# Performance work log

Hardware: AMD Instinct MI355X
Metric: run time of the kernel (lower is better)

## Reference

```python
import jax, jax.numpy as jnp
import numpy as np

S = 4096      # total packed sequence length (8 images x 512 patches)
D = 1152      # hidden_dim
H = 16        # num_heads
HD = D // H   # head_dim = 72
MLPD = 4304   # mlp_dim
EPS = 1e-5


def setup_inputs() -> dict:
    key = jax.random.key(0)
    ks = jax.random.split(key, 16)
    f32 = jnp.float32
    w = lambda k, shp: (jax.random.normal(k, shp, f32) * 0.02)
    hidden_states = jax.random.normal(ks[0], (S, D), f32)
    cu_seqlens = (jnp.arange(9, dtype=jnp.int32) * (S // 8))  # [0,512,...,4096]
    angles = jax.random.uniform(ks[1], (S, HD // 2), f32, 0.0, 2.0 * np.pi)
    rope_cos = jnp.cos(angles)
    rope_sin = jnp.sin(angles)
    return {
        "hidden_states": hidden_states,
        "cu_seqlens": cu_seqlens,
        "rope_cos": rope_cos,
        "rope_sin": rope_sin,
        "norm0_scale": jnp.ones((D,), f32),
        "norm0_bias": jnp.zeros((D,), f32),
        "wqkv_w": w(ks[2], (D, 3 * D)),
        "wqkv_b": jnp.zeros((3 * D,), f32),
        "wo_w": w(ks[3], (D, D)),
        "wo_b": jnp.zeros((D,), f32),
        "norm1_scale": jnp.ones((D,), f32),
        "norm1_bias": jnp.zeros((D,), f32),
        "fc0_w": w(ks[4], (D, MLPD)),
        "fc0_b": jnp.zeros((MLPD,), f32),
        "fc1_w": w(ks[5], (MLPD, D)),
        "fc1_b": jnp.zeros((D,), f32),
    }


def _layernorm(x, scale, bias):
    m = jnp.mean(x, axis=-1, keepdims=True)
    v = jnp.mean(jnp.square(x - m), axis=-1, keepdims=True)
    return (x - m) * jax.lax.rsqrt(v + EPS) * scale + bias


def _rope(x, cos, sin):
    # x: (S, H, HD). Complex multiply (x0 + i x1) * (cos + i sin) in real form.
    xr = x.reshape(S, H, HD // 2, 2)
    x0, x1 = xr[..., 0], xr[..., 1]
    c = cos[:, None, :]  # (S, 1, HD/2) broadcast over heads
    s = sin[:, None, :]
    o0 = x0 * c - x1 * s
    o1 = x0 * s + x1 * c
    return jnp.stack([o0, o1], axis=-1).reshape(S, H, HD)


def _block_diag_bias(cu_seqlens):
    positions = jnp.arange(S)
    starts, ends = cu_seqlens[:-1], cu_seqlens[1:]
    in_seg = (positions[:, None] >= starts[None, :]) & (positions[:, None] < ends[None, :])
    seg = jnp.argmax(in_seg.astype(jnp.int32), axis=-1)  # (S,)
    same = seg[:, None] == seg[None, :]
    return jnp.where(same, 0.0, jnp.finfo(jnp.float32).min)  # (S, S)


def reference(hidden_states, cu_seqlens, rope_cos, rope_sin,
              norm0_scale, norm0_bias, wqkv_w, wqkv_b, wo_w, wo_b,
              norm1_scale, norm1_bias, fc0_w, fc0_b, fc1_w, fc1_b):
    # pre-norm attention block
    x = _layernorm(hidden_states, norm0_scale, norm0_bias)
    qkv = (x @ wqkv_w + wqkv_b).reshape(S, 3, H, HD)
    q, k, v = qkv[:, 0], qkv[:, 1], qkv[:, 2]
    q = _rope(q, rope_cos, rope_sin)
    k = _rope(k, rope_cos, rope_sin)
    bias = _block_diag_bias(cu_seqlens)  # (S, S)
    scale = HD ** -0.5
    scores = jnp.einsum('shd,thd->hst', q, k) * scale + bias[None, :, :]
    probs = jax.nn.softmax(scores, axis=-1)
    attn = jnp.einsum('hst,thd->shd', probs, v).reshape(S, D)
    attn = attn @ wo_w + wo_b
    h = hidden_states + attn
    # pre-norm MLP block
    y = _layernorm(h, norm1_scale, norm1_bias)
    y = jax.nn.gelu(y @ fc0_w + fc0_b) @ fc1_w + fc1_b
    return h + y
```

## Files before the change

### kernel.cpp

```cpp
#include <hip/hip_runtime.h>


#define DEV __device__ __forceinline__

typedef __attribute__((ext_vector_type(8))) short short8;
typedef __attribute__((ext_vector_type(4))) float f32x4;

typedef const void __attribute__((address_space(1))) gvoid;
typedef void __attribute__((address_space(3))) lvoid;

DEV ushort f2bf(float f) {
  union { float f; unsigned u; } x; x.f = f;
  unsigned r = (x.u + 0x7FFFu + ((x.u >> 16) & 1u)) >> 16;
  return (ushort)r;
}

DEV float bf2f(ushort u) {
  union { unsigned u; float f; } x; x.u = (unsigned)u << 16;
  return x.f;
}

DEV void gload_lds16(const void* g, void* l) {
  __builtin_amdgcn_global_load_lds((gvoid*)g, (lvoid*)l, 16, 0, 0);
}

DEV f32x4 mfma16(short8 a, short8 b, f32x4 c) {
  return __builtin_amdgcn_mfma_f32_16x16x32_bf16(a, b, c, 0, 0, 0);
}

DEV float gelu_tanh(float x) {
  float x3 = x * x * x;
  return 0.5f * x * (1.f + tanhf(0.7978845608f * (x + 0.044715f * x3)));
}

__global__ void wconv_t(const float* __restrict__ src, ushort* __restrict__ dst,
                        int K, int N, int NP, int KP) {
  __shared__ float tile[32][33];
  const int k0 = blockIdx.x * 32, n0 = blockIdx.y * 32;
  const int tx = threadIdx.x & 31, ty = threadIdx.x >> 5;
#pragma unroll
  for (int i = 0; i < 4; ++i) {
    int r = ty + i * 8;
    float v = 0.f;
    if (k0 + r < K && n0 + tx < N) v = src[(size_t)(k0 + r) * N + n0 + tx];
    tile[tx][r] = v;
  }
  __syncthreads();
#pragma unroll
  for (int i = 0; i < 4; ++i) {
    int r = ty + i * 8;
    dst[(size_t)(n0 + r) * KP + k0 + tx] = f2bf(tile[r][tx]);
  }
}

__global__ __launch_bounds__(256) void ln_bf16(const float* __restrict__ x,
                                               const float* __restrict__ sc,
                                               const float* __restrict__ bi,
                                               ushort* __restrict__ out) {
  const int row = blockIdx.x, tid = threadIdx.x;
  const float* xr = x + (size_t)row * 1152;
  const int n = (tid < 128) ? 5 : 4;
  float vals[5];
  float s = 0.f, s2 = 0.f;
#pragma unroll
  for (int i = 0; i < 5; ++i) {
    if (i < n) { float v = xr[tid + i * 256]; vals[i] = v; s += v; s2 += v * v; }
  }
#pragma unroll
  for (int off = 32; off; off >>= 1) { s += __shfl_xor(s, off); s2 += __shfl_xor(s2, off); }
  __shared__ float rs[4], rs2[4];
  if ((tid & 63) == 0) { rs[tid >> 6] = s; rs2[tid >> 6] = s2; }
  __syncthreads();
  s = rs[0] + rs[1] + rs[2] + rs[3];
  s2 = rs2[0] + rs2[1] + rs2[2] + rs2[3];
  const float mean = s * (1.f / 1152.f);
  const float var = s2 * (1.f / 1152.f) - mean * mean;
  const float rstd = rsqrtf(var + 1e-5f);
  ushort* orow = out + (size_t)row * 1152;
  for (int i = 0; i < n; ++i) {
    int c = tid + i * 256;
    orow[c] = f2bf((vals[i] - mean) * rstd * sc[c] + bi[c]);
  }
}

template <int EPI, int BM>
__global__ __launch_bounds__(BM == 256 ? 512 : 256, 2) void gemm2(
    const ushort* __restrict__ A, const ushort* __restrict__ Bt,
    const float* __restrict__ bias, const float* __restrict__ resid,
    float* __restrict__ outf, ushort* __restrict__ outh,
    int N, int Kstride, int NT, int n_valid) {
  constexpr int T = BM * 2;
  constexpr int NLA = 2;
  constexpr int NLB = 512 / T;
  __shared__ ushort lA[2][BM * 32];
  __shared__ ushort lB[2][128 * 32];
  const int tid = threadIdx.x;
  const int lane = tid & 63, wave = tid >> 6;
  const int l15 = lane & 15, lg = lane >> 4;

  const int nx = gridDim.x, ny = gridDim.y;
  const int nwg = nx * ny * gridDim.z;
  const int hw = (blockIdx.z * ny + blockIdx.y) * nx + blockIdx.x;
  const int F = (hw & 7) * (nwg >> 3) + (hw >> 3);
  const int by = F % ny;
  const int C = F / ny;
  const int bx = C % nx;
  const int bz = C / nx;
  const int m0 = by * BM, n0 = bx * 128;
  const int k0 = bz * NT * 32;

  const int wm = (wave >> 1) * 64;
  const int wn = (wave & 1) * 64;

  const ushort* Asrc[NLA];
  const ushort* Bsrc[NLB];
#pragma unroll
  for (int i = 0; i < NLA; ++i) {
    const int c = i * T + tid;
    const int r = c >> 2, kc = (c & 3) ^ (r & 3);
    Asrc[i] = A + (size_t)(m0 + r) * Kstride + k0 + kc * 8;
  }
#pragma unroll
  for (int j = 0; j < NLB; ++j) {
    const int c = j * T + tid;
    const int r = c >> 2, kc = (c & 3) ^ (r & 3);
    Bsrc[j] = Bt + (size_t)(n0 + r) * Kstride + k0 + kc * 8;
  }

  auto stage = [&](int b, int t) {
#pragma unroll
    for (int i = 0; i < NLA; ++i)
      gload_lds16(Asrc[i] + t * 32, &lA[b][(i * T + wave * 64) * 8]);
#pragma unroll
    for (int j = 0; j < NLB; ++j)
      gload_lds16(Bsrc[j] + t * 32, &lB[b][(j * T + wave * 64) * 8]);
  };

  f32x4 acc[4][4] = {};
  const int cph = (lg ^ (l15 & 3)) * 8;

  stage(0, 0);
  __syncthreads();
  int cur = 0;
  for (int t = 0; t < NT; ++t) {
    if (t + 1 < NT) stage(cur ^ 1, t + 1);
    short8 af[4], bfr[4];
#pragma unroll
    for (int i = 0; i < 4; ++i)
      af[i] = *(const short8*)&lA[cur][(wm + i * 16 + l15) * 32 + cph];
#pragma unroll
    for (int j = 0; j < 4; ++j)
      bfr[j] = *(const short8*)&lB[cur][(wn + j * 16 + l15) * 32 + cph];
#pragma unroll
    for (int i = 0; i < 4; ++i)
#pragma unroll
      for (int j = 0; j < 4; ++j)
        acc[i][j] = mfma16(af[i], bfr[j], acc[i][j]);
    __syncthreads();
    cur ^= 1;
  }

  float* outp = outf;
  if constexpr (EPI == 0) outp = outf + (size_t)bz * 4096 * 1152;
  const int cb = n0 + wn + l15;
  const int rb = m0 + wm + lg * 4;
#pragma unroll
  for (int j = 0; j < 4; ++j) {
    const int col = cb + j * 16;
    const float bv = (EPI != 0 && col < n_valid) ? bias[col] : 0.f;
    const bool ok = (col < n_valid);
#pragma unroll
    for (int i = 0; i < 4; ++i) {
#pragma unroll
      for (int r = 0; r < 4; ++r) {
        const int row = rb + i * 16 + r;
        const size_t idx = (size_t)row * N + col;
        const float v = acc[i][j][r] + bv;
        if constexpr (EPI == 0) outp[idx] = v;
        else if constexpr (EPI == 1) { if (ok) outf[idx] = resid[idx] + v; }
        else if constexpr (EPI == 2) outh[idx] = f2bf(gelu_tanh(v));
        else outh[idx] = f2bf(v);
      }
    }
  }
}

__global__ __launch_bounds__(256) void ksum_reduce(
    const float* __restrict__ hb, const float* __restrict__ bias,
    const float* __restrict__ p0, const float* __restrict__ p1,
    float* __restrict__ out) {
  const f32x4* hb4 = (const f32x4*)hb;
  const f32x4* b4 = (const f32x4*)bias;
  const f32x4* p04 = (const f32x4*)p0;
  const f32x4* p14 = (const f32x4*)p1;
  f32x4* o4 = (f32x4*)out;
  const int total = 4096 * 288;
  for (int i = blockIdx.x * 256 + threadIdx.x; i < total; i += gridDim.x * 256)
    o4[i] = hb4[i] + b4[i % 288] + p04[i] + p14[i];
}

__global__ __launch_bounds__(256) void rope_pack(
    const ushort* __restrict__ qkv,
    const float* __restrict__ cosp, const float* __restrict__ sinp,
    ushort* __restrict__ qp, ushort* __restrict__ kp) {
  const int t = blockIdx.x * 256 + threadIdx.x;
  const int c = t % 12;
  const int hs = t / 12;
  const int h = hs & 15;
  const int s = hs >> 4;
  const size_t dst = ((size_t)h * 4096 + s) * 96 + c * 8;
  if (c >= 9) {
    short8 z = {};
    *(short8*)(qp + dst) = z;
    *(short8*)(kp + dst) = z;
    return;
  }
  const size_t base = (size_t)s * 3456 + h * 72 + c * 8;
  const short8 qv = *(const short8*)(qkv + base);
  const short8 kv = *(const short8*)(qkv + base + 1152);
  const f32x4 cs = *(const f32x4*)(cosp + s * 36 + c * 4);
  const f32x4 sn = *(const f32x4*)(sinp + s * 36 + c * 4);
  short8 qo, ko;
#pragma unroll
  for (int j = 0; j < 4; ++j) {
    const float q0 = bf2f((ushort)qv[2 * j]), q1 = bf2f((ushort)qv[2 * j + 1]);
    const float k0 = bf2f((ushort)kv[2 * j]), k1 = bf2f((ushort)kv[2 * j + 1]);
    qo[2 * j] = (short)f2bf((q0 * cs[j] - q1 * sn[j]) * 0.1178511302f);
    qo[2 * j + 1] = (short)f2bf((q0 * sn[j] + q1 * cs[j]) * 0.1178511302f);
    ko[2 * j] = (short)f2bf(k0 * cs[j] - k1 * sn[j]);
    ko[2 * j + 1] = (short)f2bf(k0 * sn[j] + k1 * cs[j]);
  }
  *(short8*)(qp + dst) = qo;
  *(short8*)(kp + dst) = ko;
}

__global__ void v_pack(const ushort* __restrict__ qkv, ushort* __restrict__ vt) {
  __shared__ ushort lv[96][64];
  const int b = blockIdx.x;
  const int h = b >> 6;
  const int s0 = (b & 63) << 6;
  const int tid = threadIdx.x;
#pragma unroll
  for (int it = 0; it < 24; ++it) {
    int idx = tid + it * 256;
    int d = idx % 96, sl = idx / 96;
    lv[d][sl] = (d < 72) ? qkv[(size_t)(s0 + sl) * 3456 + 2304 + h * 72 + d] : (ushort)0;
  }
  __syncthreads();
#pragma unroll
  for (int it = 0; it < 24; ++it) {
    int idx = tid + it * 256;
    int d = idx >> 6, sl = idx & 63;
    vt[((size_t)h * 96 + d) * 4096 + s0 + sl] = lv[d][sl];
  }
}

__global__ __launch_bounds__(256) void attn_kernel(
    const ushort* __restrict__ qp, const ushort* __restrict__ kp,
    const ushort* __restrict__ vt, ushort* __restrict__ attn_out) {
  __shared__ ushort lp[4][16 * 32];
  const int tid = threadIdx.x, lane = tid & 63, wave = tid >> 6;
  const int l15 = lane & 15, lg = lane >> 4;
  const int b = blockIdx.x;
  const int h = b >> 6;
  const int rem = b & 63;
  const int seg = rem >> 3, qt = rem & 7;
  const int q0 = seg * 512 + qt * 64 + wave * 16;

  short8 aq[3];
  const ushort* qrow = qp + ((size_t)h * 4096 + q0 + l15) * 96 + lg * 8;
  aq[0] = *(const short8*)(qrow);
  aq[1] = *(const short8*)(qrow + 32);
  aq[2] = *(const short8*)(qrow + 64);

  f32x4 oacc[5] = {};
  float mrow[4] = {-1e30f, -1e30f, -1e30f, -1e30f};
  float srow[4] = {0.f, 0.f, 0.f, 0.f};

  const ushort* kbase = kp + ((size_t)h * 4096 + seg * 512) * 96;
  const ushort* vbase = vt + (size_t)h * 96 * 4096 + seg * 512;
  ushort* lpw = lp[wave];

  for (int kc = 0; kc < 16; ++kc) {
    f32x4 sc[2] = {};
#pragma unroll
    for (int n = 0; n < 2; ++n) {
      const ushort* krow = kbase + (size_t)(kc * 32 + n * 16 + l15) * 96 + lg * 8;
#pragma unroll
      for (int c = 0; c < 3; ++c) {
        short8 kb = *(const short8*)(krow + c * 32);
        sc[n] = mfma16(aq[c], kb, sc[n]);
      }
    }
    float corr[4];
#pragma unroll
    for (int j = 0; j < 4; ++j) {
      float v = fmaxf(sc[0][j], sc[1][j]);
      v = fmaxf(v, __shfl_xor(v, 1));
      v = fmaxf(v, __shfl_xor(v, 2));
      v = fmaxf(v, __shfl_xor(v, 4));
      v = fmaxf(v, __shfl_xor(v, 8));
      float mn = fmaxf(mrow[j], v);
      corr[j] = __expf(mrow[j] - mn);
      mrow[j] = mn;
    }
    float p0[4], p1[4];
#pragma unroll
    for (int j = 0; j < 4; ++j) {
      p0[j] = __expf(sc[0][j] - mrow[j]);
      p1[j] = __expf(sc[1][j] - mrow[j]);
      float ps = p0[j] + p1[j];
      ps += __shfl_xor(ps, 1);
      ps += __shfl_xor(ps, 2);
      ps += __shfl_xor(ps, 4);
      ps += __shfl_xor(ps, 8);
      srow[j] = srow[j] * corr[j] + ps;
    }
#pragma unroll
    for (int n = 0; n < 5; ++n)
#pragma unroll
      for (int j = 0; j < 4; ++j)
        oacc[n][j] *= corr[j];
#pragma unroll
    for (int j = 0; j < 4; ++j) {
      int row = lg * 4 + j;
      lpw[row * 32 + l15] = f2bf(p0[j]);
      lpw[row * 32 + 16 + l15] = f2bf(p1[j]);
    }
    __syncthreads();
    short8 pa = *(const short8*)&lpw[l15 * 32 + lg * 8];
    const ushort* vrow = vbase + kc * 32 + lg * 8;
#pragma unroll
    for (int n = 0; n < 5; ++n) {
      short8 vb = *(const short8*)(vrow + (size_t)(n * 16 + l15) * 4096);
      oacc[n] = mfma16(pa, vb, oacc[n]);
    }
    __syncthreads();
  }
#pragma unroll
  for (int j = 0; j < 4; ++j) {
    float inv = 1.f / srow[j];
    int row = q0 + lg * 4 + j;
#pragma unroll
    for (int n = 0; n < 5; ++n) {
      int col = n * 16 + l15;
      if (col < 72)
        attn_out[(size_t)row * 1152 + h * 72 + col] = f2bf(oacc[n][j] * inv);
    }
  }
}

extern "C" void kernel_launch(void* const* d_in, const int* in_sizes, int n_in,
                              void* d_out, int out_size, void* d_ws, size_t ws_size,
                              hipStream_t stream) {
  (void)in_sizes; (void)n_in; (void)out_size;
  const float* hidden = (const float*)d_in[0];
  const float* ropec = (const float*)d_in[2];
  const float* ropes = (const float*)d_in[3];
  const float* n0s = (const float*)d_in[4];
  const float* n0b = (const float*)d_in[5];
  const float* wqkv = (const float*)d_in[6];
  const float* bqkv = (const float*)d_in[7];
  const float* wo = (const float*)d_in[8];
  const float* bo = (const float*)d_in[9];
  const float* n1s = (const float*)d_in[10];
  const float* n1b = (const float*)d_in[11];
  const float* wfc0 = (const float*)d_in[12];
  const float* bfc0 = (const float*)d_in[13];
  const float* wfc1 = (const float*)d_in[14];
  const float* bfc1 = (const float*)d_in[15];
  float* out = (float*)d_out;

  char* ws = (char*)d_ws;
  ushort* x_bf   = (ushort*)(ws + 0);
  ushort* wqkv_t = (ushort*)(ws + 9437184);
  ushort* wo_t   = (ushort*)(ws + 17399808);
  ushort* fc0_t  = (ushort*)(ws + 20054016);
  ushort* fc1_t  = (ushort*)(ws + 30081024);
  ushort* qkv_bf = (ushort*)(ws + 40108032);
  ushort* mid    = (ushort*)(ws + 40108032);
  ushort* q_pad  = (ushort*)(ws + 75759616);
  ushort* k_pad  = (ushort*)(ws + 88342528);
  ushort* vt     = (ushort*)(ws + 100925440);
  float*  pbuf   = (float*)(ws + 75759616);
  ushort* attn   = (ushort*)(ws + 113508352);
  float*  hbuf   = (float*)(ws + 122945536);
  ushort* yln    = (ushort*)(ws + 141819904);
  if (ws_size < 151257088) return;

  wconv_t<<<dim3(36, 108), 256, 0, stream>>>(wqkv, wqkv_t, 1152, 3456, 3456, 1152);
  wconv_t<<<dim3(36, 36), 256, 0, stream>>>(wo, wo_t, 1152, 1152, 1152, 1152);
  wconv_t<<<dim3(36, 136), 256, 0, stream>>>(wfc0, fc0_t, 1152, 4304, 4352, 1152);
  wconv_t<<<dim3(136, 36), 256, 0, stream>>>(wfc1, fc1_t, 4304, 1152, 1152, 4352);

  ln_bf16<<<4096, 256, 0, stream>>>(hidden, n0s, n0b, x_bf);

  gemm2<3, 256><<<dim3(27, 16), 512, 0, stream>>>(x_bf, wqkv_t, bqkv, nullptr, nullptr, qkv_bf,
                                                  3456, 1152, 36, 3456);
  rope_pack<<<3072, 256, 0, stream>>>(qkv_bf, ropec, ropes, q_pad, k_pad);
  v_pack<<<1024, 256, 0, stream>>>(qkv_bf, vt);

  attn_kernel<<<1024, 256, 0, stream>>>(q_pad, k_pad, vt, attn);

  gemm2<1, 128><<<dim3(9, 32), 256, 0, stream>>>(attn, wo_t, bo, hidden, hbuf, nullptr,
                                                 1152, 1152, 36, 1152);
  ln_bf16<<<4096, 256, 0, stream>>>(hbuf, n1s, n1b, yln);

  gemm2<2, 256><<<dim3(34, 16), 512, 0, stream>>>(yln, fc0_t, bfc0, nullptr, nullptr, mid,
                                                  4352, 1152, 36, 4304);
  gemm2<0, 128><<<dim3(9, 32, 2), 256, 0, stream>>>(mid, fc1_t, nullptr, nullptr, pbuf, nullptr,
                                                    1152, 4352, 68, 1152);
  ksum_reduce<<<2048, 256, 0, stream>>>(hbuf, bfc1, pbuf, pbuf + (size_t)4096 * 1152, out);
}
```

Measured before the change: 371.1 us.

## Replace double-buffered GEMM with single-buffer 128x128 tile kernel at higher occupancy

Replaces the templated double-buffered GEMM, which used 256-row tiles for the QKV and FC0 projections, with a single-buffered 128x128 kernel. It uses a new paired-row XOR swizzle in LDS and launch bounds allowing three workgroups per CU. All four GEMMs now use 128-row tiles, which doubles the grid for QKV and FC0. The goal is to hide memory latency through occupancy instead of in-kernel prefetch, at the cost of losing load/compute overlap within a workgroup and re-reading operands more often. The column guard in the residual epilogue is also dropped, since N equals n_valid there.

```diff
diff --git a/kernel.cpp b/kernel.cpp
--- a/kernel.cpp
+++ b/kernel.cpp
@@ -83,20 +83,18 @@
   }
 }
 
-template <int EPI, int BM>
-__global__ __launch_bounds__(BM == 256 ? 512 : 256, 2) void gemm2(
+template <int EPI>
+__global__ __launch_bounds__(256, 3) void gemmS(
     const ushort* __restrict__ A, const ushort* __restrict__ Bt,
     const float* __restrict__ bias, const float* __restrict__ resid,
     float* __restrict__ outf, ushort* __restrict__ outh,
     int N, int Kstride, int NT, int n_valid) {
-  constexpr int T = BM * 2;
-  constexpr int NLA = 2;
-  constexpr int NLB = 512 / T;
-  __shared__ ushort lA[2][BM * 32];
-  __shared__ ushort lB[2][128 * 32];
+  __shared__ ushort lA[4096];
+  __shared__ ushort lB[4096];
   const int tid = threadIdx.x;
   const int lane = tid & 63, wave = tid >> 6;
   const int l15 = lane & 15, lg = lane >> 4;
+  const int wm = (wave >> 1) * 64, wn = (wave & 1) * 64;
 
   const int nx = gridDim.x, ny = gridDim.y;
   const int nwg = nx * ny * gridDim.z;
@@ -106,58 +104,54 @@
   const int C = F / ny;
   const int bx = C % nx;
   const int bz = C / nx;
-  const int m0 = by * BM, n0 = bx * 128;
+  const int m0 = by * 128, n0 = bx * 128;
   const int k0 = bz * NT * 32;
 
-  const int wm = (wave >> 1) * 64;
-  const int wn = (wave & 1) * 64;
-
-  const ushort* Asrc[NLA];
-  const ushort* Bsrc[NLB];
-#pragma unroll
-  for (int i = 0; i < NLA; ++i) {
-    const int c = i * T + tid;
-    const int r = c >> 2, kc = (c & 3) ^ (r & 3);
-    Asrc[i] = A + (size_t)(m0 + r) * Kstride + k0 + kc * 8;
-  }
-#pragma unroll
-  for (int j = 0; j < NLB; ++j) {
-    const int c = j * T + tid;
-    const int r = c >> 2, kc = (c & 3) ^ (r & 3);
-    Bsrc[j] = Bt + (size_t)(n0 + r) * Kstride + k0 + kc * 8;
-  }
-
-  auto stage = [&](int b, int t) {
-#pragma unroll
-    for (int i = 0; i < NLA; ++i)
-      gload_lds16(Asrc[i] + t * 32, &lA[b][(i * T + wave * 64) * 8]);
-#pragma unroll
-    for (int j = 0; j < NLB; ++j)
-      gload_lds16(Bsrc[j] + t * 32, &lB[b][(j * T + wave * 64) * 8]);
-  };
+  const ushort* sA0;
+  const ushort* sA1;
+  const ushort* sB0;
+  const ushort* sB1;
+  {
+    const int r2a = tid >> 3, inva = (tid & 7) ^ (r2a & 7);
+    const int r2b = 32 + r2a;
+    sA0 = A + (size_t)(m0 + r2a * 2 + (inva >> 2)) * Kstride + k0 + (inva & 3) * 8;
+    sA1 = A + (size_t)(m0 + r2b * 2 + (inva >> 2)) * Kstride + k0 + (inva & 3) * 8;
+    sB0 = Bt + (size_t)(n0 + r2a * 2 + (inva >> 2)) * Kstride + k0 + (inva & 3) * 8;
+    sB1 = Bt + (size_t)(n0 + r2b * 2 + (inva >> 2)) * Kstride + k0 + (inva & 3) * 8;
+  }
+
+  int offA[4], offB[4];
+#pragma unroll
+  for (int f = 0; f < 4; ++f) {
+    const int rA = wm + f * 16 + l15;
+    const int r2 = rA >> 1, c8 = ((((rA & 1) << 2) | lg)) ^ (r2 & 7);
+    offA[f] = (r2 * 8 + c8) * 8;
+    const int rB = wn + f * 16 + l15;
+    const int s2 = rB >> 1, d8 = ((((rB & 1) << 2) | lg)) ^ (s2 & 7);
+    offB[f] = (s2 * 8 + d8) * 8;
+  }
 
   f32x4 acc[4][4] = {};
-  const int cph = (lg ^ (l15 & 3)) * 8;
-
-  stage(0, 0);
-  __syncthreads();
-  int cur = 0;
+
   for (int t = 0; t < NT; ++t) {
-    if (t + 1 < NT) stage(cur ^ 1, t + 1);
+    const int ko = t * 32;
+    gload_lds16(sA0 + ko, &lA[tid * 8]);
+    gload_lds16(sA1 + ko, &lA[2048 + tid * 8]);
+    gload_lds16(sB0 + ko, &lB[tid * 8]);
+    gload_lds16(sB1 + ko, &lB[2048 + tid * 8]);
+    __syncthreads();
     short8 af[4], bfr[4];
 #pragma unroll
-    for (int i = 0; i < 4; ++i)
-      af[i] = *(const short8*)&lA[cur][(wm + i * 16 + l15) * 32 + cph];
-#pragma unroll
-    for (int j = 0; j < 4; ++j)
-      bfr[j] = *(const short8*)&lB[cur][(wn + j * 16 + l15) * 32 + cph];
+    for (int f = 0; f < 4; ++f) {
+      af[f] = *(const short8*)&lA[offA[f]];
+      bfr[f] = *(const short8*)&lB[offB[f]];
+    }
 #pragma unroll
     for (int i = 0; i < 4; ++i)
 #pragma unroll
       for (int j = 0; j < 4; ++j)
         acc[i][j] = mfma16(af[i], bfr[j], acc[i][j]);
     __syncthreads();
-    cur ^= 1;
   }
 
   float* outp = outf;
@@ -168,7 +162,6 @@
   for (int j = 0; j < 4; ++j) {
     const int col = cb + j * 16;
     const float bv = (EPI != 0 && col < n_valid) ? bias[col] : 0.f;
-    const bool ok = (col < n_valid);
 #pragma unroll
     for (int i = 0; i < 4; ++i) {
 #pragma unroll
@@ -177,7 +170,7 @@
         const size_t idx = (size_t)row * N + col;
         const float v = acc[i][j][r] + bv;
         if constexpr (EPI == 0) outp[idx] = v;
-        else if constexpr (EPI == 1) { if (ok) outf[idx] = resid[idx] + v; }
+        else if constexpr (EPI == 1) outf[idx] = resid[idx] + v;
         else if constexpr (EPI == 2) outh[idx] = f2bf(gelu_tanh(v));
         else outh[idx] = f2bf(v);
       }
@@ -395,20 +388,20 @@
 
   ln_bf16<<<4096, 256, 0, stream>>>(hidden, n0s, n0b, x_bf);
 
-  gemm2<3, 256><<<dim3(27, 16), 512, 0, stream>>>(x_bf, wqkv_t, bqkv, nullptr, nullptr, qkv_bf,
-                                                  3456, 1152, 36, 3456);
+  gemmS<3><<<dim3(27, 32), 256, 0, stream>>>(x_bf, wqkv_t, bqkv, nullptr, nullptr, qkv_bf,
+                                             3456, 1152, 36, 3456);
   rope_pack<<<3072, 256, 0, stream>>>(qkv_bf, ropec, ropes, q_pad, k_pad);
   v_pack<<<1024, 256, 0, stream>>>(qkv_bf, vt);
 
   attn_kernel<<<1024, 256, 0, stream>>>(q_pad, k_pad, vt, attn);
 
-  gemm2<1, 128><<<dim3(9, 32), 256, 0, stream>>>(attn, wo_t, bo, hidden, hbuf, nullptr,
-                                                 1152, 1152, 36, 1152);
+  gemmS<1><<<dim3(9, 32), 256, 0, stream>>>(attn, wo_t, bo, hidden, hbuf, nullptr,
+                                            1152, 1152, 36, 1152);
   ln_bf16<<<4096, 256, 0, stream>>>(hbuf, n1s, n1b, yln);
 
-  gemm2<2, 256><<<dim3(34, 16), 512, 0, stream>>>(yln, fc0_t, bfc0, nullptr, nullptr, mid,
-                                                  4352, 1152, 36, 4304);
-  gemm2<0, 128><<<dim3(9, 32, 2), 256, 0, stream>>>(mid, fc1_t, nullptr, nullptr, pbuf, nullptr,
-                                                    1152, 4352, 68, 1152);
+  gemmS<2><<<dim3(34, 32), 256, 0, stream>>>(yln, fc0_t, bfc0, nullptr, nullptr, mid,
+                                             4352, 1152, 36, 4304);
+  gemmS<0><<<dim3(9, 32, 2), 256, 0, stream>>>(mid, fc1_t, nullptr, nullptr, pbuf, nullptr,
+                                               1152, 4352, 68, 1152);
   ksum_reduce<<<2048, 256, 0, stream>>>(hbuf, bfc1, pbuf, pbuf + (size_t)4096 * 1152, out);
 }
```

Result: no change. 371.5 us (+0.1%).
